# Optimization experiments

Hardware: AMD Instinct MI355X
Metric: run time of the kernel (lower is better)

## Reference

```python
import jax, jax.numpy as jnp
import numpy as np

VOCAB, EMBED, HIDDEN = 32000, 512, 1024
B, T = 2, 2048
LN_EPS = 1e-5


def setup_inputs() -> dict:
    key = jax.random.key(0)
    ks = jax.random.split(key, 12)

    def xavier(k, fan_in, fan_out):
        lim = float(np.sqrt(6.0 / (fan_in + fan_out)))
        return jax.random.uniform(k, (fan_in, fan_out), jnp.float32, -lim, lim)

    return {
        "tokens": jax.random.randint(ks[0], (B, T), 0, VOCAB),
        "E": xavier(ks[1], VOCAB, EMBED),                    # embedding table
        "Wc": xavier(ks[2], EMBED, HIDDEN),                  # fc_current (stored [in,out])
        "bc": jnp.full((HIDDEN,), 0.01, jnp.float32),
        "Wh": xavier(ks[3], EMBED, HIDDEN),                  # fc_context
        "bh": jnp.full((HIDDEN,), 0.01, jnp.float32),
        "Wm": xavier(ks[4], 2 * HIDDEN, HIDDEN),             # fc_merge
        "bm": jnp.full((HIDDEN,), 0.01, jnp.float32),
        "Wo": xavier(ks[5], HIDDEN, VOCAB),                  # fc_out
        "bo": jnp.full((VOCAB,), 0.01, jnp.float32),
        "ln_w": jnp.ones((HIDDEN,), jnp.float32),
        "ln_b": jnp.zeros((HIDDEN,), jnp.float32),
    }


def reference(tokens, E, Wc, bc, Wh, bh, Wm, bm, Wo, bo, ln_w, ln_b):
    emb = E[tokens]  # [B, T, D]
    # history mean at step t = mean(emb[:, :t]); at t==0 the module uses current embed
    csum = jnp.cumsum(emb, axis=1)
    counts = jnp.arange(1, T, dtype=emb.dtype)[None, :, None]
    hist_mean = jnp.concatenate([emb[:, :1], csum[:, :-1] / counts], axis=1)  # [B,T,D]

    cur_enc = jax.nn.relu(jnp.einsum("btd,dh->bth", emb, Wc) + bc)
    hist_enc = jax.nn.relu(jnp.einsum("btd,dh->bth", hist_mean, Wh) + bh)
    merged = jnp.concatenate([cur_enc, hist_enc], axis=-1)  # [B,T,2H]
    merged = jax.nn.relu(jnp.einsum("btk,kh->bth", merged, Wm) + bm)

    mu = jnp.mean(merged, axis=-1, keepdims=True)
    var = jnp.mean(jnp.square(merged - mu), axis=-1, keepdims=True)
    normed = (merged - mu) * jax.lax.rsqrt(var + LN_EPS) * ln_w + ln_b

    logits = (jnp.einsum("bth,hv->btv", normed, Wo) + bo) / 10.0  # [B,T,V]
    return logits
```

## Files before the change

kernel.cpp:

```cpp
#include <hip/hip_runtime.h>
#include <hip/hip_bf16.h>
#include <stdint.h>
#include <stdio.h>

#define T_SEQ  2048
#define BATCH  2
#define NROWS  4096
#define EMBED  512
#define HIDDEN 1024
#define VOCAB  32000
#define NCHUNK 32
#define CHLEN  64

typedef __bf16 bf16x8 __attribute__((ext_vector_type(8)));
typedef float  f32x4  __attribute__((ext_vector_type(4)));

__device__ __forceinline__ float b2f(unsigned short h) {
  union { unsigned int u; float f; } v; v.u = ((unsigned int)h) << 16; return v.f;
}
__device__ __forceinline__ unsigned short f2b(float f) {
  union { float f; unsigned int u; } v; v.f = f;
  unsigned int u = v.u;
  u += 0x7fffu + ((u >> 16) & 1u);
  return (unsigned short)(u >> 16);
}

__global__ void gather_kernel(const int* __restrict__ tokens,
                              const float* __restrict__ E,
                              unsigned short* __restrict__ emb) {
  const int row = blockIdx.x;
  const int tok = tokens[row];
  const float2 v = ((const float2*)(E + (size_t)tok * EMBED))[threadIdx.x];
  const uint32_t packed = (uint32_t)f2b(v.x) | ((uint32_t)f2b(v.y) << 16);
  ((uint32_t*)(emb + (size_t)row * EMBED))[threadIdx.x] = packed;
}

__global__ void scan_sum_kernel(const unsigned short* __restrict__ emb,
                                float* __restrict__ csum) {
  const int bc = blockIdx.x;
  const int d  = threadIdx.x;
  const unsigned short* e = emb + ((size_t)bc * CHLEN) * EMBED + d;
  float s = 0.f;
  #pragma unroll 8
  for (int i = 0; i < CHLEN; ++i) s += b2f(e[(size_t)i * EMBED]);
  csum[(size_t)bc * EMBED + d] = s;
}

__global__ void scan_excl_kernel(float* __restrict__ csum) {
  const int b = blockIdx.x;
  const int d = threadIdx.x;
  float run = 0.f;
  for (int c = 0; c < NCHUNK; ++c) {
    const size_t idx = ((size_t)b * NCHUNK + c) * EMBED + d;
    const float v = csum[idx];
    csum[idx] = run;
    run += v;
  }
}

__global__ void scan_emit_kernel(const unsigned short* __restrict__ emb,
                                 const float* __restrict__ csum,
                                 unsigned short* __restrict__ hist) {
  const int bc = blockIdx.x;
  const int c  = bc & (NCHUNK - 1);
  const int d  = threadIdx.x;
  const unsigned short* e = emb  + ((size_t)bc * CHLEN) * EMBED + d;
  unsigned short*       h = hist + ((size_t)bc * CHLEN) * EMBED + d;
  float sum = csum[(size_t)bc * EMBED + d];
  #pragma unroll 8
  for (int i = 0; i < CHLEN; ++i) {
    const int t = c * CHLEN + i;
    h[(size_t)i * EMBED] = (t == 0) ? e[0] : f2b(sum / (float)t);
    sum += b2f(e[(size_t)i * EMBED]);
  }
}

__global__ void transpose_cast_kernel(const float* __restrict__ in,
                                      unsigned short* __restrict__ out,
                                      int R, int C) {
  __shared__ float tile[32][33];
  const int tx = threadIdx.x & 31;
  const int ty = threadIdx.x >> 5;
  const int r0 = blockIdx.y * 32, c0 = blockIdx.x * 32;
  #pragma unroll
  for (int i = 0; i < 32; i += 8)
    tile[ty + i][tx] = in[(size_t)(r0 + ty + i) * C + (c0 + tx)];
  __syncthreads();
  #pragma unroll
  for (int i = 0; i < 32; i += 8)
    out[(size_t)(c0 + ty + i) * R + (r0 + tx)] = f2b(tile[tx][ty + i]);
}

#define BM 128
#define BN 128
#define BK 32

__device__ __forceinline__ void async16(unsigned short* lds, const unsigned short* g) {
  __builtin_amdgcn_global_load_lds(
      (const __attribute__((address_space(1))) void*)g,
      (__attribute__((address_space(3))) void*)lds, 16, 0, 0);
}

template<int MODE>
__global__ __launch_bounds__(256) void gemm_bt_kernel(
    const unsigned short* __restrict__ A,
    const unsigned short* __restrict__ BT,
    const float* __restrict__ bias,
    void* __restrict__ out, int M, int N, int K, int ldOut, int colOff,
    const unsigned short* __restrict__ A2,
    const unsigned short* __restrict__ BT2,
    const float* __restrict__ bias2, int colOff2) {
  __shared__ unsigned short As[BM * BK];
  __shared__ unsigned short Bs[BN * BK];

  const unsigned short* Ap = A;
  const unsigned short* Bp = BT;
  const float*          bp = bias;
  int                   co = colOff;
  if (blockIdx.z) { Ap = A2; Bp = BT2; bp = bias2; co = colOff2; }

  int wg = blockIdx.x;
  {
    const int nwg = gridDim.x;
    const int xcd = wg & 7, loc = wg >> 3;
    const int q = nwg >> 3, r = nwg & 7;
    wg = (xcd < r ? xcd * (q + 1) : r * (q + 1) + (xcd - r) * q) + loc;
  }
  const int nmb = M / BM;
  const int mb  = wg % nmb;
  const int nb  = wg / nmb;
  const int m0  = mb * BM;
  const int n0  = nb * BN;

  const int tid  = threadIdx.x;
  const int wave = tid >> 6;
  const int lane = tid & 63;
  const int wm = (wave & 1) * 64;
  const int wn = (wave >> 1) * 64;

  const int srow = (wave << 5) + (lane >> 2);
  const int scol = (lane & 3) << 3;
  const unsigned short* aSrc = Ap + (size_t)(m0 + srow) * K + scol;
  const unsigned short* bSrc = Bp + (size_t)(n0 + srow) * K + scol;
  unsigned short* aDst = As + (wave << 5) * BK;
  unsigned short* bDst = Bs + (wave << 5) * BK;

  f32x4 acc[4][4];
  #pragma unroll
  for (int i = 0; i < 4; ++i)
    #pragma unroll
    for (int j = 0; j < 4; ++j)
      acc[i][j] = (f32x4){0.f, 0.f, 0.f, 0.f};

  const int q = lane >> 4;
  const int r = lane & 15;

  for (int k0 = 0; k0 < K; k0 += BK) {
    __syncthreads();
    async16(aDst,           aSrc);
    async16(aDst + 16 * BK, aSrc + 16 * (size_t)K);
    async16(bDst,           bSrc);
    async16(bDst + 16 * BK, bSrc + 16 * (size_t)K);
    aSrc += BK; bSrc += BK;
    __syncthreads();

    bf16x8 af[4], bfr[4];
    #pragma unroll
    for (int mi = 0; mi < 4; ++mi)
      af[mi] = *(const bf16x8*)&As[(wm + mi * 16 + r) * BK + (q << 3)];
    #pragma unroll
    for (int ni = 0; ni < 4; ++ni)
      bfr[ni] = *(const bf16x8*)&Bs[(wn + ni * 16 + r) * BK + (q << 3)];
    #pragma unroll
    for (int mi = 0; mi < 4; ++mi)
      #pragma unroll
      for (int ni = 0; ni < 4; ++ni)
        acc[mi][ni] = __builtin_amdgcn_mfma_f32_16x16x32_bf16(
            af[mi], bfr[ni], acc[mi][ni], 0, 0, 0);
  }

  #pragma unroll
  for (int ni = 0; ni < 4; ++ni) {
    const int col = n0 + wn + ni * 16 + r;
    const float bv = bp[col];
    #pragma unroll
    for (int mi = 0; mi < 4; ++mi) {
      #pragma unroll
      for (int e = 0; e < 4; ++e) {
        const int row = m0 + wm + mi * 16 + (q << 2) + e;
        float v = acc[mi][ni][e] + bv;
        if (MODE == 0 || MODE == 1) v = fmaxf(v, 0.f);
        if (MODE == 2) v *= 0.1f;
        const size_t idx = (size_t)row * ldOut + co + col;
        if (MODE == 0)      ((unsigned short*)out)[idx] = f2b(v);
        else if (MODE == 1) ((float*)out)[idx] = v;
        else                __builtin_nontemporal_store(v, &((float*)out)[idx]);
      }
    }
  }
}

__global__ void ln_kernel(const float* __restrict__ merged,
                          const float* __restrict__ lnw,
                          const float* __restrict__ lnb,
                          unsigned short* __restrict__ normed) {
  const int row = blockIdx.x;
  const float4 v = ((const float4*)(merged + (size_t)row * HIDDEN))[threadIdx.x];
  float s  = v.x + v.y + v.z + v.w;
  float ss = v.x * v.x + v.y * v.y + v.z * v.z + v.w * v.w;
  #pragma unroll
  for (int off = 32; off > 0; off >>= 1) {
    s  += __shfl_down(s, off, 64);
    ss += __shfl_down(ss, off, 64);
  }
  __shared__ float red[8];
  const int wvi = threadIdx.x >> 6;
  if ((threadIdx.x & 63) == 0) { red[wvi] = s; red[4 + wvi] = ss; }
  __syncthreads();
  s  = red[0] + red[1] + red[2] + red[3];
  ss = red[4] + red[5] + red[6] + red[7];
  const float mu  = s * (1.0f / HIDDEN);
  const float var = ss * (1.0f / HIDDEN) - mu * mu;
  const float rs  = rsqrtf(var + 1e-5f);
  const float4 w4 = ((const float4*)lnw)[threadIdx.x];
  const float4 b4 = ((const float4*)lnb)[threadIdx.x];
  ushort4 o;
  o.x = f2b((v.x - mu) * rs * w4.x + b4.x);
  o.y = f2b((v.y - mu) * rs * w4.y + b4.y);
  o.z = f2b((v.z - mu) * rs * w4.z + b4.z);
  o.w = f2b((v.w - mu) * rs * w4.w + b4.w);
  ((ushort4*)(normed + (size_t)row * HIDDEN))[threadIdx.x] = o;
}

extern "C" void kernel_launch(void* const* d_in, const int* in_sizes, int n_in,
                              void* d_out, int out_size, void* d_ws, size_t ws_size,
                              hipStream_t stream) {
  const int*   tokens = (const int*)d_in[0];
  const float* E      = (const float*)d_in[1];
  const float* Wc     = (const float*)d_in[2];
  const float* bc     = (const float*)d_in[3];
  const float* Wh     = (const float*)d_in[4];
  const float* bh     = (const float*)d_in[5];
  const float* Wm     = (const float*)d_in[6];
  const float* bm     = (const float*)d_in[7];
  const float* Wo     = (const float*)d_in[8];
  const float* bo     = (const float*)d_in[9];
  const float* lnw    = (const float*)d_in[10];
  const float* lnb    = (const float*)d_in[11];

  char* p = (char*)d_ws;
  unsigned short* WcT  = (unsigned short*)p; p += (size_t)HIDDEN * EMBED * 2;
  unsigned short* WhT  = (unsigned short*)p; p += (size_t)HIDDEN * EMBED * 2;
  unsigned short* WmT  = (unsigned short*)p; p += (size_t)HIDDEN * (2 * HIDDEN) * 2;
  unsigned short* WoT  = (unsigned short*)p; p += (size_t)VOCAB * HIDDEN * 2;
  unsigned short* emb  = (unsigned short*)p; p += (size_t)NROWS * EMBED * 2;
  unsigned short* hist = (unsigned short*)p; p += (size_t)NROWS * EMBED * 2;
  unsigned short* cat  = (unsigned short*)p; p += (size_t)NROWS * (2 * HIDDEN) * 2;
  float*          mrg  = (float*)p;          p += (size_t)NROWS * HIDDEN * 4;
  unsigned short* nrm  = (unsigned short*)p; p += (size_t)NROWS * HIDDEN * 2;
  float*          csum = (float*)p;          p += (size_t)BATCH * NCHUNK * EMBED * 4;
  if ((size_t)(p - (char*)d_ws) > ws_size)
    fprintf(stderr, "WS TOO SMALL: need %zu have %zu\n", (size_t)(p - (char*)d_ws), ws_size);

  transpose_cast_kernel<<<dim3(HIDDEN / 32, EMBED / 32), 256, 0, stream>>>(Wc, WcT, EMBED, HIDDEN);
  transpose_cast_kernel<<<dim3(HIDDEN / 32, EMBED / 32), 256, 0, stream>>>(Wh, WhT, EMBED, HIDDEN);
  transpose_cast_kernel<<<dim3(HIDDEN / 32, (2 * HIDDEN) / 32), 256, 0, stream>>>(Wm, WmT, 2 * HIDDEN, HIDDEN);
  transpose_cast_kernel<<<dim3(VOCAB / 32, HIDDEN / 32), 256, 0, stream>>>(Wo, WoT, HIDDEN, VOCAB);

  gather_kernel<<<NROWS, 256, 0, stream>>>(tokens, E, emb);
  scan_sum_kernel <<<BATCH * NCHUNK, EMBED, 0, stream>>>(emb, csum);
  scan_excl_kernel<<<BATCH, EMBED, 0, stream>>>(csum);
  scan_emit_kernel<<<BATCH * NCHUNK, EMBED, 0, stream>>>(emb, csum, hist);

  const int nwgEnc = (NROWS / BM) * (HIDDEN / BN);
  const int nwgOut = (NROWS / BM) * (VOCAB / BN);

  gemm_bt_kernel<0><<<dim3(nwgEnc, 1, 2), 256, 0, stream>>>(
      emb, WcT, bc, cat, NROWS, HIDDEN, EMBED, 2 * HIDDEN, 0,
      hist, WhT, bh, HIDDEN);
  gemm_bt_kernel<1><<<dim3(nwgEnc, 1, 1), 256, 0, stream>>>(
      cat, WmT, bm, mrg, NROWS, HIDDEN, 2 * HIDDEN, HIDDEN, 0,
      nullptr, nullptr, nullptr, 0);
  ln_kernel<<<NROWS, 256, 0, stream>>>(mrg, lnw, lnb, nrm);
  gemm_bt_kernel<2><<<dim3(nwgOut, 1, 1), 256, 0, stream>>>(
      nrm, WoT, bo, d_out, NROWS, VOCAB, HIDDEN, VOCAB, 0,
      nullptr, nullptr, nullptr, 0);
}
```

Baseline: 1.080 ms.

## Add 256x256 double-buffered output GEMM kernel with XCD-aware tile remapping

Replaces the 128x128 GEMM used for the vocabulary projection with a dedicated kernel. It uses 256x256 tiles, 8 waves and XOR-swizzled LDS. Loads are double-buffered asynchronously and staged in quarters interleaved with MFMA phases, with setprio hints and a remap of workgroups across XCDs. The aim is higher arithmetic intensity and better overlap of global loads with matrix math on the dominant GEMM. It also drops nontemporal stores for the logits and relies on K being a multiple of 128 and M, N being multiples of 256.

```diff
diff --git a/kernel.cpp b/kernel.cpp
--- a/kernel.cpp
+++ b/kernel.cpp
@@ -91,15 +91,15 @@
     out[(size_t)(c0 + ty + i) * R + (r0 + tx)] = f2b(tile[tx][ty + i]);
 }
 
-#define BM 128
-#define BN 128
-#define BK 32
-
 __device__ __forceinline__ void async16(unsigned short* lds, const unsigned short* g) {
   __builtin_amdgcn_global_load_lds(
       (const __attribute__((address_space(1))) void*)g,
       (__attribute__((address_space(3))) void*)lds, 16, 0, 0);
 }
+
+#define BM 128
+#define BN 128
+#define BK 32
 
 template<int MODE>
 __global__ __launch_bounds__(256) void gemm_bt_kernel(
@@ -192,10 +192,180 @@
         if (MODE == 0 || MODE == 1) v = fmaxf(v, 0.f);
         if (MODE == 2) v *= 0.1f;
         const size_t idx = (size_t)row * ldOut + co + col;
-        if (MODE == 0)      ((unsigned short*)out)[idx] = f2b(v);
-        else if (MODE == 1) ((float*)out)[idx] = v;
-        else                __builtin_nontemporal_store(v, &((float*)out)[idx]);
+        if (MODE == 0) ((unsigned short*)out)[idx] = f2b(v);
+        else           ((float*)out)[idx] = v;
       }
+    }
+  }
+}
+
+
+#define BAR() do {                            \
+    asm volatile("" ::: "memory");            \
+    __builtin_amdgcn_sched_barrier(0);        \
+    __builtin_amdgcn_s_barrier();             \
+    __builtin_amdgcn_sched_barrier(0);        \
+    asm volatile("" ::: "memory");            \
+  } while (0)
+
+__global__ __launch_bounds__(512, 2) void gemm256_out_kernel(
+    const unsigned short* __restrict__ A,
+    const unsigned short* __restrict__ BT,
+    const float* __restrict__ bias,
+    float* __restrict__ out, int M, int N, int K, int ldOut) {
+  __shared__ unsigned short lds[2][2][2][8192];
+
+  int wg = blockIdx.x;
+  {
+    const int nwg = gridDim.x;
+    const int xcd = wg & 7, loc = wg >> 3;
+    const int q8 = nwg >> 3, r8 = nwg & 7;
+    wg = (xcd < r8 ? xcd * (q8 + 1) : r8 * (q8 + 1) + (xcd - r8) * q8) + loc;
+  }
+  const int nmb = M >> 8;
+  const int mb = wg % nmb, nb = wg / nmb;
+  const int m0 = mb << 8, n0 = nb << 8;
+
+  const int tid  = threadIdx.x;
+  const int wave = tid >> 6, lane = tid & 63;
+  const int wr = wave >> 2, wc = wave & 3;
+  const int q = lane >> 4, r = lane & 15, rr = lane & 7;
+
+  const int srow = (wave << 4) + (lane >> 3);
+  const int scol = ((lane & 7) ^ (lane >> 3)) << 3;
+  const unsigned short* aB = A  + (size_t)(m0 + srow) * K + scol;
+  const unsigned short* bB = BT + (size_t)(n0 + srow) * K + scol;
+
+  const int NTt = K >> 6;
+
+  auto stage = [&](int matB, int h, int tb, int kt) {
+    unsigned short* d = &lds[tb][matB][h][wave << 10];
+    const unsigned short* s =
+        (matB ? bB : aB) + (size_t)h * 128 * K + ((size_t)kt << 6);
+    async16(d, s);
+    async16(d + 512, s + ((size_t)K << 3));
+  };
+
+  auto ldA = [&](int tb, int mi, int ks) {
+    return *(const bf16x8*)&lds[tb][0][wr]
+        [(mi * 16 + r) * 64 + ((((ks << 2) | q) ^ rr) << 3)];
+  };
+  auto ldB = [&](int tb, int ni, int ks) {
+    return *(const bf16x8*)&lds[tb][1][wc >> 1]
+        [(((wc & 1) << 6) + ni * 16 + r) * 64 + ((((ks << 2) | q) ^ rr) << 3)];
+  };
+
+  f32x4 acc[8][4];
+  #pragma unroll
+  for (int i = 0; i < 8; ++i)
+    #pragma unroll
+    for (int j = 0; j < 4; ++j)
+      acc[i][j] = (f32x4){0.f, 0.f, 0.f, 0.f};
+
+  bf16x8 afr[8][2], bfr[2][2];
+
+  stage(0, 0, 0, 0); stage(0, 1, 0, 0); stage(1, 0, 0, 0); stage(1, 1, 0, 0);
+  if (NTt > 1) {
+    stage(0, 0, 1, 1); stage(0, 1, 1, 1); stage(1, 0, 1, 1);
+    asm volatile("s_waitcnt vmcnt(6)" ::: "memory");
+  } else {
+    asm volatile("s_waitcnt vmcnt(0)" ::: "memory");
+  }
+  BAR();
+
+#define TILE(U, BU) do {                                                       \
+    const int u_ = (U);                                                        \
+                            \
+    _Pragma("unroll")                                                          \
+    for (int mi = 0; mi < 4; ++mi) {                                           \
+      afr[mi][0] = ldA(BU, mi, 0); afr[mi][1] = ldA(BU, mi, 1);                \
+    }                                                                          \
+    _Pragma("unroll")                                                          \
+    for (int nj = 0; nj < 2; ++nj) {                                           \
+      bfr[nj][0] = ldB(BU, nj, 0); bfr[nj][1] = ldB(BU, nj, 1);                \
+    }                                                                          \
+    if (u_ + 1 < NTt) stage(1, 1, 1 - (BU), u_ + 1);                           \
+    __builtin_amdgcn_s_setprio(1);                                             \
+    _Pragma("unroll")                                                          \
+    for (int mi = 0; mi < 4; ++mi)                                             \
+      _Pragma("unroll")                                                        \
+      for (int nj = 0; nj < 2; ++nj) {                                         \
+        acc[mi][nj] = __builtin_amdgcn_mfma_f32_16x16x32_bf16(                 \
+            afr[mi][0], bfr[nj][0], acc[mi][nj], 0, 0, 0);                     \
+        acc[mi][nj] = __builtin_amdgcn_mfma_f32_16x16x32_bf16(                 \
+            afr[mi][1], bfr[nj][1], acc[mi][nj], 0, 0, 0);                     \
+      }                                                                        \
+    __builtin_amdgcn_s_setprio(0);                                             \
+    BAR();                                                                     \
+                                 \
+    _Pragma("unroll")                                                          \
+    for (int mi = 4; mi < 8; ++mi) {                                           \
+      afr[mi][0] = ldA(BU, mi, 0); afr[mi][1] = ldA(BU, mi, 1);                \
+    }                                                                          \
+    __builtin_amdgcn_s_setprio(1);                                             \
+    _Pragma("unroll")                                                          \
+    for (int mi = 4; mi < 8; ++mi)                                             \
+      _Pragma("unroll")                                                        \
+      for (int nj = 0; nj < 2; ++nj) {                                         \
+        acc[mi][nj] = __builtin_amdgcn_mfma_f32_16x16x32_bf16(                 \
+            afr[mi][0], bfr[nj][0], acc[mi][nj], 0, 0, 0);                     \
+        acc[mi][nj] = __builtin_amdgcn_mfma_f32_16x16x32_bf16(                 \
+            afr[mi][1], bfr[nj][1], acc[mi][nj], 0, 0, 0);                     \
+      }                                                                        \
+    __builtin_amdgcn_s_setprio(0);                                             \
+    BAR();                                                                     \
+                            \
+    _Pragma("unroll")                                                          \
+    for (int nj = 0; nj < 2; ++nj) {                                           \
+      bfr[nj][0] = ldB(BU, 2 + nj, 0); bfr[nj][1] = ldB(BU, 2 + nj, 1);        \
+    }                                                                          \
+    if (u_ + 2 < NTt) stage(0, 0, BU, u_ + 2);                                 \
+    __builtin_amdgcn_s_setprio(1);                                             \
+    _Pragma("unroll")                                                          \
+    for (int mi = 0; mi < 4; ++mi)                                             \
+      _Pragma("unroll")                                                        \
+      for (int nj = 0; nj < 2; ++nj) {                                         \
+        acc[mi][2 + nj] = __builtin_amdgcn_mfma_f32_16x16x32_bf16(             \
+            afr[mi][0], bfr[nj][0], acc[mi][2 + nj], 0, 0, 0);                 \
+        acc[mi][2 + nj] = __builtin_amdgcn_mfma_f32_16x16x32_bf16(             \
+            afr[mi][1], bfr[nj][1], acc[mi][2 + nj], 0, 0, 0);                 \
+      }                                                                        \
+    __builtin_amdgcn_s_setprio(0);                                             \
+    BAR();                                                                     \
+                   \
+    if (u_ + 2 < NTt) { stage(0, 1, BU, u_ + 2); stage(1, 0, BU, u_ + 2); }    \
+    __builtin_amdgcn_s_setprio(1);                                             \
+    _Pragma("unroll")                                                          \
+    for (int mi = 4; mi < 8; ++mi)                                             \
+      _Pragma("unroll")                                                        \
+      for (int nj = 0; nj < 2; ++nj) {                                         \
+        acc[mi][2 + nj] = __builtin_amdgcn_mfma_f32_16x16x32_bf16(             \
+            afr[mi][0], bfr[nj][0], acc[mi][2 + nj], 0, 0, 0);                 \
+        acc[mi][2 + nj] = __builtin_amdgcn_mfma_f32_16x16x32_bf16(             \
+            afr[mi][1], bfr[nj][1], acc[mi][2 + nj], 0, 0, 0);                 \
+      }                                                                        \
+    __builtin_amdgcn_s_setprio(0);                                             \
+    if (u_ + 2 < NTt) asm volatile("s_waitcnt vmcnt(6)" ::: "memory");         \
+    else              asm volatile("s_waitcnt vmcnt(0)" ::: "memory");         \
+    BAR();                                                                     \
+  } while (0)
+
+  for (int u = 0; u < NTt; u += 2) {
+    TILE(u, 0);
+    TILE(u + 1, 1);
+  }
+#undef TILE
+
+  #pragma unroll
+  for (int ni = 0; ni < 4; ++ni) {
+    const int col = n0 + (wc << 6) + ni * 16 + r;
+    const float bv = bias[col];
+    #pragma unroll
+    for (int mi = 0; mi < 8; ++mi) {
+      const int row = m0 + (wr << 7) + mi * 16 + (q << 2);
+      #pragma unroll
+      for (int e = 0; e < 4; ++e)
+        out[(size_t)(row + e) * ldOut + col] = (acc[mi][ni][e] + bv) * 0.1f;
     }
   }
 }
@@ -273,7 +443,6 @@
   scan_emit_kernel<<<BATCH * NCHUNK, EMBED, 0, stream>>>(emb, csum, hist);
 
   const int nwgEnc = (NROWS / BM) * (HIDDEN / BN);
-  const int nwgOut = (NROWS / BM) * (VOCAB / BN);
 
   gemm_bt_kernel<0><<<dim3(nwgEnc, 1, 2), 256, 0, stream>>>(
       emb, WcT, bc, cat, NROWS, HIDDEN, EMBED, 2 * HIDDEN, 0,
@@ -282,7 +451,8 @@
       cat, WmT, bm, mrg, NROWS, HIDDEN, 2 * HIDDEN, HIDDEN, 0,
       nullptr, nullptr, nullptr, 0);
   ln_kernel<<<NROWS, 256, 0, stream>>>(mrg, lnw, lnb, nrm);
-  gemm_bt_kernel<2><<<dim3(nwgOut, 1, 1), 256, 0, stream>>>(
-      nrm, WoT, bo, d_out, NROWS, VOCAB, HIDDEN, VOCAB, 0,
-      nullptr, nullptr, nullptr, 0);
-}
+
+  const int nwgOut = (NROWS / 256) * (VOCAB / 256);
+  gemm256_out_kernel<<<dim3(nwgOut), 512, 0, stream>>>(
+      nrm, WoT, bo, (float*)d_out, NROWS, VOCAB, HIDDEN, VOCAB);
+}
```

New measurement: 1.049 ms. -2.9%, faster.
